# Kernel optimization log

Measured on AMD Instinct MI355X. Metric: run time of the kernel, lower is better.

The kernel has to match this reference:

```python
import jax, jax.numpy as jnp
import numpy as np

HIDDEN = 2048
NH = 32        # query heads
NKV = 4        # kv heads (GQA)
HD = 64        # head_dim
Q_SIZE = NH * HD      # 2048
KV_SIZE = NKV * HD    # 256
WINDOW = 1024         # sliding window size
THETA = 1000000.0
T = 2048              # tokens
SCALE = HD ** -0.5
NEG = -1e30


def setup_inputs() -> dict:
    key = jax.random.key(0)
    k1, k2, k3 = jax.random.split(key, 3)
    return {
        "positions": jnp.arange(T, dtype=jnp.int32),
        "hidden_states": jax.random.normal(k1, (T, HIDDEN), dtype=jnp.float32),
        "wqkv": jax.random.normal(k2, (HIDDEN, Q_SIZE + 2 * KV_SIZE), dtype=jnp.float32) * (HIDDEN ** -0.5),
        "wo": jax.random.normal(k3, (Q_SIZE, HIDDEN), dtype=jnp.float32) * (Q_SIZE ** -0.5),
    }


def _apply_rope(x, positions):
    # NeoX-style rotary embedding over full head_dim (rotate halves).
    half = HD // 2
    inv_freq = 1.0 / (THETA ** (jnp.arange(half, dtype=jnp.float32) / half))
    ang = positions.astype(jnp.float32)[:, None] * inv_freq[None, :]   # [T, half]
    cos = jnp.cos(ang)[:, None, :]   # [T, 1, half]
    sin = jnp.sin(ang)[:, None, :]
    x1, x2 = jnp.split(x, 2, axis=-1)
    return jnp.concatenate([x1 * cos - x2 * sin, x2 * cos + x1 * sin], axis=-1)


def reference(positions, hidden_states, wqkv, wo):
    # fused QKV projection
    qkv = hidden_states @ wqkv                          # [T, Q+2KV]
    q = qkv[:, :Q_SIZE].reshape(T, NH, HD)
    k = qkv[:, Q_SIZE:Q_SIZE + KV_SIZE].reshape(T, NKV, HD)
    v = qkv[:, Q_SIZE + KV_SIZE:].reshape(T, NKV, HD)
    # rotary embedding on q, k
    q = _apply_rope(q, positions)
    k = _apply_rope(k, positions)
    # GQA: repeat kv heads to match query heads
    group = NH // NKV
    kr = jnp.repeat(k, group, axis=1)                   # [T, NH, HD]
    vr = jnp.repeat(v, group, axis=1)
    scores = jnp.einsum('qhd,khd->hqk', q, kr) * SCALE  # [NH, T, T]
    # causal + sliding-window mask: attend to j in (i-WINDOW, i]
    i = jnp.arange(T)[:, None]
    j = jnp.arange(T)[None, :]
    mask = (j <= i) & (i - j < WINDOW)                  # [T, T]
    scores = jnp.where(mask[None, :, :], scores, NEG)
    probs = jax.nn.softmax(scores, axis=-1)
    attn = jnp.einsum('hqk,khd->qhd', probs, vr).reshape(T, Q_SIZE)
    return attn @ wo                                    # [T, HIDDEN]
```

## Files before the change

### kernel.cpp

```cpp
#include <hip/hip_runtime.h>
#include <hip/hip_bf16.h>

typedef float  f32x4  __attribute__((ext_vector_type(4)));
typedef __bf16 bf16x8 __attribute__((ext_vector_type(8)));
typedef __bf16 bf16x4 __attribute__((ext_vector_type(4)));
typedef __bf16 bf16x2 __attribute__((ext_vector_type(2)));

#define T_SEQ   2048
#define HIDDEN  2048
#define NH      32
#define NKV     4
#define HD      64
#define QSZ     2048
#define KVSZ    256
#define QKVN    2560
#define WINDOW  1024

#if __has_builtin(__builtin_amdgcn_exp2f)
#define EXPS(x) __builtin_amdgcn_exp2f(x)
#define QSCALE  0.1803368801111f
#else
#define EXPS(x) __expf(x)
#define QSCALE  0.125f
#endif

#define RAW_BARRIER()   asm volatile("s_barrier" ::: "memory")
#define WAITV(n)        asm volatile("s_waitcnt vmcnt(" #n ")" ::: "memory")

__device__ __forceinline__ void gll16(const __bf16* g, __bf16* l) {
    __builtin_amdgcn_global_load_lds(
        (const __attribute__((address_space(1))) void*)g,
        (__attribute__((address_space(3))) void*)l,
        16, 0, 0);
}

__global__ __launch_bounds__(256) void prep(const float4* __restrict__ hidden4,
                                            bf16x4* __restrict__ hidden_bf4,
                                            const float* __restrict__ wqkv,
                                            const float* __restrict__ wo,
                                            __bf16* __restrict__ wqkv_t,
                                            __bf16* __restrict__ wo_t,
                                            const int* __restrict__ pos,
                                            float2* __restrict__ ropetab) {
    __shared__ float tile[32][132];
    const int b = blockIdx.x;
    const int tid = threadIdx.x;

    if (b < 4096) {
        int id = b * 256 + tid;
        float4 v = hidden4[id];
        bf16x4 o;
        o[0] = (__bf16)v.x; o[1] = (__bf16)v.y; o[2] = (__bf16)v.z; o[3] = (__bf16)v.w;
        hidden_bf4[id] = o;
        return;
    }
    if (b < 4352) {
        int id = (b - 4096) * 256 + tid;
        int row = id >> 5, f = id & 31;
        float p = (float)pos[row];
        float ifr = exp2f((float)f * -0.62286151779138f);
        float sn, cs;
        sincosf(p * ifr, &sn, &cs);
        ropetab[id] = make_float2(cs, sn);
        return;
    }

    const float* in;
    __bf16* out;
    int Rin, Cin, bx, by;
    if (b < 5632) {
        int t = b - 4352;
        in = wqkv; out = wqkv_t; Rin = 2048; Cin = 2560;
        bx = t % 20; by = t / 20;
    } else {
        int t = b - 5632;
        in = wo; out = wo_t; Rin = 2048; Cin = 2048;
        bx = t % 16; by = t / 16;
    }
    const int ri = by * 32, ci = bx * 128;
    const int r0 = tid >> 5;
    const int c4 = tid & 31;
    #pragma unroll
    for (int i = 0; i < 4; i++) {
        float4 v = *reinterpret_cast<const float4*>(
            &in[(size_t)(ri + r0 + i * 8) * Cin + ci + c4 * 4]);
        *reinterpret_cast<float4*>(&tile[r0 + i * 8][c4 * 4]) = v;
    }
    __syncthreads();
    const int c  = tid >> 3;
    const int rb = tid & 7;
    #pragma unroll
    for (int j = 0; j < 4; j++) {
        int cc = c + j * 32;
        bf16x4 pk;
        #pragma unroll
        for (int i = 0; i < 4; i++) pk[i] = (__bf16)tile[rb * 4 + i][cc];
        *reinterpret_cast<bf16x4*>(&out[(size_t)(ci + cc) * Rin + ri + rb * 4]) = pk;
    }
}


#define GEMM_PROLOGUE_COMMON(Aptr, Btptr, Kdim)                                 \
    const int tid = threadIdx.x;                                                \
    const int wid = tid >> 6;                                                   \
    const int l   = tid & 63;                                                   \
    const int lg  = l >> 4;                                                     \
    const int ll  = l & 15;                                                     \
    const int swl = ll & 7;                                                     \
    const int wm  = wid >> 1, wn = wid & 1;                                     \
    const int gx   = gridDim.x;                                                 \
    const int flat = blockIdx.y * gx + blockIdx.x;                              \
    const int nwg  = gx * gridDim.y;                                            \
    const int swz  = (flat & 7) * (nwg >> 3) + (flat >> 3);                     \
    const int bm   = (swz / gx) * 64;                                           \
    const int bn   = (swz % gx) * 128;                                          \
    const __bf16* Ab = (Aptr) + (size_t)bm * (Kdim);                            \
    const __bf16* Bb = (Btptr) + (size_t)bn * (Kdim);                           \
    f32x4 acc[2][4];                                                            \
    _Pragma("unroll")                                                           \
    for (int i = 0; i < 2; i++)                                                 \
        _Pragma("unroll")                                                       \
        for (int j = 0; j < 4; j++)                                             \
            acc[i][j] = (f32x4){0.f, 0.f, 0.f, 0.f};                            \
    const int srow = tid >> 3;                                                  \
    const int sseg0 = tid & 7;

#define GEMM_STAGE(buf, k0, Kdim)                                               \
    {                                                                           \
        _Pragma("unroll")                                                       \
        for (int c = 0; c < 2; c++) {                                           \
            int row  = c * 32 + srow;                                           \
            int sseg = sseg0 ^ (row & 7);                                       \
            gll16(Ab + (size_t)row * (Kdim) + (k0) + sseg * 8,                  \
                  &Asm[buf][(c * 256 + tid) * 8]);                              \
        }                                                                       \
        _Pragma("unroll")                                                       \
        for (int c = 0; c < 4; c++) {                                           \
            int row  = c * 32 + srow;                                           \
            int sseg = sseg0 ^ (row & 7);                                       \
            gll16(Bb + (size_t)row * (Kdim) + (k0) + sseg * 8,                  \
                  &Bsm[buf][(c * 256 + tid) * 8]);                              \
        }                                                                       \
    }

#define GEMM_COMPUTE(bufidx)                                                    \
    _Pragma("unroll")                                                           \
    for (int ss = 0; ss < 2; ss++) {                                            \
        bf16x8 af[2], bfr[4];                                                   \
        _Pragma("unroll")                                                       \
        for (int mi = 0; mi < 2; mi++) {                                        \
            int r = wm * 32 + mi * 16 + ll;                                     \
            int u = (ss * 4 + lg) ^ swl;                                        \
            af[mi] = *reinterpret_cast<const bf16x8*>(&Asm[bufidx][r * 64 + u * 8]); \
        }                                                                       \
        _Pragma("unroll")                                                       \
        for (int ni = 0; ni < 4; ni++) {                                        \
            int r = wn * 64 + ni * 16 + ll;                                     \
            int u = (ss * 4 + lg) ^ swl;                                        \
            bfr[ni] = *reinterpret_cast<const bf16x8*>(&Bsm[bufidx][r * 64 + u * 8]); \
        }                                                                       \
        _Pragma("unroll")                                                       \
        for (int mi = 0; mi < 2; mi++)                                          \
            _Pragma("unroll")                                                   \
            for (int ni = 0; ni < 4; ni++)                                      \
                acc[mi][ni] = __builtin_amdgcn_mfma_f32_16x16x32_bf16(          \
                    af[mi], bfr[ni], acc[mi][ni], 0, 0, 0);                     \
    }

#define GEMM_KLOOP2(Kdim)                                                       \
    GEMM_STAGE(0, 0, Kdim)                                                      \
    int cur = 0;                                                                \
    for (int k0 = 0; k0 < (Kdim); k0 += 64) {                                   \
        RAW_BARRIER();                                                          \
        if (k0 + 64 < (Kdim)) {                                                 \
            GEMM_STAGE(cur ^ 1, k0 + 64, Kdim)                                  \
            WAITV(6);                                                           \
        } else {                                                                \
            WAITV(0);                                                           \
        }                                                                       \
        RAW_BARRIER();                                                          \
        __builtin_amdgcn_sched_barrier(0);                                      \
        GEMM_COMPUTE(cur)                                                       \
        cur ^= 1;                                                               \
    }

#define GEMM_KLOOP3(Kdim)                                                       \
    GEMM_STAGE(0, 0, Kdim)                                                      \
    GEMM_STAGE(1, 64, Kdim)                                                     \
    int cur = 0;                                                                \
    for (int k0 = 0; k0 < (Kdim); k0 += 64) {                                   \
        if (k0 + 64 < (Kdim)) { WAITV(6); } else { WAITV(0); }                  \
        RAW_BARRIER();                                                          \
        __builtin_amdgcn_sched_barrier(0);                                      \
        if (k0 + 128 < (Kdim)) {                                                \
            int nb = cur + 2; if (nb >= 3) nb -= 3;                             \
            GEMM_STAGE(nb, k0 + 128, Kdim)                                      \
        }                                                                       \
        GEMM_COMPUTE(cur)                                                       \
        cur = (cur == 2) ? 0 : cur + 1;                                         \
    }

__global__ __launch_bounds__(256) void gemm_out(const __bf16* __restrict__ A,
                                                const __bf16* __restrict__ Bt,
                                                float* __restrict__ Cout,
                                                int M, int N, int K) {
    __shared__ __align__(16) __bf16 Asm[3][64 * 64];
    __shared__ __align__(16) __bf16 Bsm[3][128 * 64];
    GEMM_PROLOGUE_COMMON(A, Bt, K)
    GEMM_KLOOP3(K)
    #pragma unroll
    for (int mi = 0; mi < 2; mi++)
        #pragma unroll
        for (int ni = 0; ni < 4; ni++)
            #pragma unroll
            for (int r = 0; r < 4; r++) {
                int row = bm + wm*32 + mi*16 + lg*4 + r;
                int col = bn + wn*64 + ni*16 + ll;
                Cout[(size_t)row * N + col] = acc[mi][ni][r];
            }
}

__global__ __launch_bounds__(256) void gemm_qkv(const __bf16* __restrict__ A,
                                                const __bf16* __restrict__ Bt,
                                                const float2* __restrict__ ropetab,
                                                __bf16* __restrict__ q,
                                                __bf16* __restrict__ k,
                                                __bf16* __restrict__ vT) {
    __shared__ __align__(16) __bf16 Asm[2][64 * 64];
    __shared__ __align__(16) __bf16 Bsm[2][128 * 64];
    GEMM_PROLOGUE_COMMON(A, Bt, HIDDEN)
    GEMM_KLOOP2(HIDDEN)

    if (bn < QSZ + KVSZ) {
        const bool isq = (bn < QSZ);
        #pragma unroll
        for (int mi = 0; mi < 2; mi++) {
            #pragma unroll
            for (int r = 0; r < 4; r++) {
                int row = bm + wm*32 + mi*16 + lg*4 + r;
                const float2* tb = &ropetab[row * 32 + ll];
                #pragma unroll
                for (int ni = 0; ni < 2; ni++) {
                    float2 cssn = tb[ni * 16];
                    float x1 = acc[mi][ni][r], x2 = acc[mi][ni + 2][r];
                    float o1 = x1 * cssn.x - x2 * cssn.y;
                    float o2 = x2 * cssn.x + x1 * cssn.y;
                    int col = bn + wn*64 + ni*16 + ll;
                    if (isq) {
                        q[(size_t)row * QSZ + col]      = (__bf16)(o1 * QSCALE);
                        q[(size_t)row * QSZ + col + 32] = (__bf16)(o2 * QSCALE);
                    } else {
                        k[(size_t)row * KVSZ + (col - QSZ)]      = (__bf16)o1;
                        k[(size_t)row * KVSZ + (col - QSZ) + 32] = (__bf16)o2;
                    }
                }
            }
        }
    } else {
        #pragma unroll
        for (int mi = 0; mi < 2; mi++) {
            int row0 = bm + wm*32 + mi*16 + lg*4;
            #pragma unroll
            for (int ni = 0; ni < 4; ni++) {
                int d = bn + wn*64 + ni*16 + ll - (QSZ + KVSZ);
                bf16x4 pk;
                #pragma unroll
                for (int r = 0; r < 4; r++) pk[r] = (__bf16)acc[mi][ni][r];
                *reinterpret_cast<bf16x4*>(&vT[(size_t)d * T_SEQ + row0]) = pk;
            }
        }
    }
}

__global__ __launch_bounds__(512) void attn_kernel(const __bf16* __restrict__ qg,
                                                   const __bf16* __restrict__ kgl,
                                                   const __bf16* __restrict__ vTg,
                                                   __bf16* __restrict__ og) {
    const int qb  = blockIdx.x;
    const int hp  = blockIdx.y;
    const int kvh = hp >> 2;
    const int tid = threadIdx.x;
    const int wid = tid >> 6;
    const int h   = hp * 2 + (wid >> 2);
    const int l   = tid & 63;
    const int lg  = l >> 4;
    const int ll  = l & 15;
    const int i0  = qb * 64;
    const int qw  = i0 + (wid & 3) * 16;
    const int qi  = qw + ll;

    __shared__ __align__(16) __bf16 Ksm[3][64 * 64];
    __shared__ __align__(16) __bf16 VTs[3][64 * 64];

    bf16x8 qf[2];
    {
        const __bf16* qp = qg + (size_t)(qw + ll) * QSZ + h * 64 + lg * 8;
        qf[0] = *reinterpret_cast<const bf16x8*>(qp);
        qf[1] = *reinterpret_cast<const bf16x8*>(qp + 32);
    }

    f32x4 o[4];
    #pragma unroll
    for (int dn = 0; dn < 4; dn++) o[dn] = (f32x4){0.f, 0.f, 0.f, 0.f};
    float l_run = 0.f;

    int jlo = i0 - (WINDOW - 1); if (jlo < 0) jlo = 0;
    int t0v = jlo & ~63;
    int tend = i0 + 64;

    const int srow = tid >> 3;
    const int sg   = (tid & 7) ^ (srow & 7);
    const int krow = (srow & 35) | ((srow & 8) << 1) | ((srow & 4) << 1) | ((srow & 16) >> 2);
    const __bf16* kp = kgl + (size_t)krow * KVSZ + kvh * 64 + sg * 8;
    const __bf16* vp = vTg + (size_t)(kvh * 64 + srow) * T_SEQ + sg * 8;

#define ASTAGE(buf, t)                                      \
    {                                                       \
        gll16(kp + (size_t)(t) * KVSZ, &Ksm[buf][tid * 8]); \
        gll16(vp + (t),                &VTs[buf][tid * 8]); \
    }

    ASTAGE(0, t0v);
    if (t0v + 64 < tend) ASTAGE(1, t0v + 64);

    const int swl = ll & 7;
    const int u0 = (lg ^ swl) * 8;
    const int u1 = ((4 + lg) ^ swl) * 8;

    int cur = 0;
    for (int t = t0v; t < tend; t += 64) {
        if (t + 64 < tend) { WAITV(2); } else { WAITV(0); }
        RAW_BARRIER();
        __builtin_amdgcn_sched_barrier(0);
        if (t + 128 < tend) {
            int nb = cur + 2; if (nb >= 3) nb -= 3;
            ASTAGE(nb, t + 128);
        }

        bool active = (t <= qw + 15) && (t + 63 >= qw - (WINDOW - 1));
        if (active) {
            f32x4 sT[4];
            __builtin_amdgcn_s_setprio(1);
            #pragma unroll
            for (int kt = 0; kt < 4; kt++) {
                sT[kt] = (f32x4){0.f, 0.f, 0.f, 0.f};
                bf16x8 kf0 = *reinterpret_cast<const bf16x8*>(&Ksm[cur][kt*1024 + ll*64 + u0]);
                sT[kt] = __builtin_amdgcn_mfma_f32_16x16x32_bf16(kf0, qf[0], sT[kt], 0, 0, 0);
                bf16x8 kf1 = *reinterpret_cast<const bf16x8*>(&Ksm[cur][kt*1024 + ll*64 + u1]);
                sT[kt] = __builtin_amdgcn_mfma_f32_16x16x32_bf16(kf1, qf[1], sT[kt], 0, 0, 0);
            }
            __builtin_amdgcn_s_setprio(0);

            bool full = (t + 63 <= qw) && (t >= qw + 15 - (WINDOW - 1));
            float ts = 0.f;
            if (full) {
                #pragma unroll
                for (int kt = 0; kt < 4; kt++) {
                    #pragma unroll
                    for (int r = 0; r < 4; r++) {
                        float p = EXPS(sT[kt][r]);
                        sT[kt][r] = p;
                        ts += p;
                    }
                }
            } else {
                #pragma unroll
                for (int kt = 0; kt < 4; kt++) {
                    int jb = t + ((kt & 2) << 4) + ((kt & 1) << 2) + (lg << 3);
                    #pragma unroll
                    for (int r = 0; r < 4; r++) {
                        int j = jb + r;
                        bool ok = (j <= qi) && (qi - j < WINDOW);
                        float p = ok ? EXPS(sT[kt][r]) : 0.f;
                        sT[kt][r] = p;
                        ts += p;
                    }
                }
            }
            ts += __shfl_xor(ts, 16);
            ts += __shfl_xor(ts, 32);
            l_run += ts;

            __builtin_amdgcn_s_setprio(1);
            #pragma unroll
            for (int kt2 = 0; kt2 < 2; kt2++) {
                bf16x8 pa;
                #pragma unroll
                for (int r = 0; r < 4; r++) {
                    pa[r]     = (__bf16)sT[kt2*2][r];
                    pa[r + 4] = (__bf16)sT[kt2*2 + 1][r];
                }
                int uv = kt2 ? u1 : u0;
                #pragma unroll
                for (int dn = 0; dn < 4; dn++) {
                    bf16x8 vf = *reinterpret_cast<const bf16x8*>(&VTs[cur][dn*1024 + ll*64 + uv]);
                    o[dn] = __builtin_amdgcn_mfma_f32_16x16x32_bf16(pa, vf, o[dn], 0, 0, 0);
                }
            }
            __builtin_amdgcn_s_setprio(0);
        }
        cur = (cur == 2) ? 0 : cur + 1;
    }
#undef ASTAGE

    float linv = 1.0f / l_run;
    float i0v = __shfl(linv, lg*4 + 0);
    float i1v = __shfl(linv, lg*4 + 1);
    float i2v = __shfl(linv, lg*4 + 2);
    float i3v = __shfl(linv, lg*4 + 3);
    #pragma unroll
    for (int dn = 0; dn < 4; dn++) {
        og[(size_t)(qw + lg*4 + 0) * QSZ + h*64 + dn*16 + ll] = (__bf16)(o[dn][0] * i0v);
        og[(size_t)(qw + lg*4 + 1) * QSZ + h*64 + dn*16 + ll] = (__bf16)(o[dn][1] * i1v);
        og[(size_t)(qw + lg*4 + 2) * QSZ + h*64 + dn*16 + ll] = (__bf16)(o[dn][2] * i2v);
        og[(size_t)(qw + lg*4 + 3) * QSZ + h*64 + dn*16 + ll] = (__bf16)(o[dn][3] * i3v);
    }
}

extern "C" void kernel_launch(void* const* d_in, const int* in_sizes, int n_in,
                              void* d_out, int out_size, void* d_ws, size_t ws_size,
                              hipStream_t stream) {
    const int*   positions = (const int*)d_in[0];
    const float* hidden    = (const float*)d_in[1];
    const float* wqkv      = (const float*)d_in[2];
    const float* wo        = (const float*)d_in[3];
    float* out = (float*)d_out;

    char* ws = (char*)d_ws;
    __bf16* hidden_bf = (__bf16*)(ws);
    __bf16* wqkv_t    = (__bf16*)(ws + 8388608);
    __bf16* wo_t      = (__bf16*)(ws + 18874368);
    __bf16* q_bf      = (__bf16*)(ws + 37748736);
    __bf16* k_bf      = (__bf16*)(ws + 46137344);
    __bf16* vT_bf     = (__bf16*)(ws + 47185920);
    __bf16* attn_bf   = (__bf16*)(ws + 48234496);
    float2* ropetab   = (float2*)(ws + 56623104);

    prep<<<dim3(6656), dim3(256), 0, stream>>>(
        (const float4*)hidden, (bf16x4*)hidden_bf, wqkv, wo,
        wqkv_t, wo_t, positions, ropetab);

    gemm_qkv<<<dim3(QKVN / 128, T_SEQ / 64), dim3(256), 0, stream>>>(
        hidden_bf, wqkv_t, ropetab, q_bf, k_bf, vT_bf);

    attn_kernel<<<dim3(T_SEQ / 64, 16), dim3(512), 0, stream>>>(
        q_bf, k_bf, vT_bf, attn_bf);

    gemm_out<<<dim3(HIDDEN / 128, T_SEQ / 64), dim3(256), 0, stream>>>(
        attn_bf, wo_t, out, T_SEQ, HIDDEN, QSZ);
}
```

Measured before the change: 106.1 us.

## Move wo transpose-convert into attention launch as extra blocks

The wo fp32-to-bf16 transpose leaves the prep kernel and runs as 1024 extra blocks appended to the attention grid. The attention kernel now uses one flat grid and a shared memory buffer that both roles carve up. The aim is to overlap the bandwidth-bound weight conversion with compute-bound attention and shorten the prep launch. The risk is that the extra blocks compete for CUs with attention blocks and change the tail behaviour.

```diff
diff --git a/kernel.cpp b/kernel.cpp
--- a/kernel.cpp
+++ b/kernel.cpp
@@ -37,9 +37,7 @@
 __global__ __launch_bounds__(256) void prep(const float4* __restrict__ hidden4,
                                             bf16x4* __restrict__ hidden_bf4,
                                             const float* __restrict__ wqkv,
-                                            const float* __restrict__ wo,
                                             __bf16* __restrict__ wqkv_t,
-                                            __bf16* __restrict__ wo_t,
                                             const int* __restrict__ pos,
                                             float2* __restrict__ ropetab) {
     __shared__ float tile[32][132];
@@ -65,25 +63,15 @@
         return;
     }
 
-    const float* in;
-    __bf16* out;
-    int Rin, Cin, bx, by;
-    if (b < 5632) {
-        int t = b - 4352;
-        in = wqkv; out = wqkv_t; Rin = 2048; Cin = 2560;
-        bx = t % 20; by = t / 20;
-    } else {
-        int t = b - 5632;
-        in = wo; out = wo_t; Rin = 2048; Cin = 2048;
-        bx = t % 16; by = t / 16;
-    }
+    int t = b - 4352;
+    const int bx = t % 20, by = t / 20;
     const int ri = by * 32, ci = bx * 128;
     const int r0 = tid >> 5;
     const int c4 = tid & 31;
     #pragma unroll
     for (int i = 0; i < 4; i++) {
         float4 v = *reinterpret_cast<const float4*>(
-            &in[(size_t)(ri + r0 + i * 8) * Cin + ci + c4 * 4]);
+            &wqkv[(size_t)(ri + r0 + i * 8) * QKVN + ci + c4 * 4]);
         *reinterpret_cast<float4*>(&tile[r0 + i * 8][c4 * 4]) = v;
     }
     __syncthreads();
@@ -95,7 +83,7 @@
         bf16x4 pk;
         #pragma unroll
         for (int i = 0; i < 4; i++) pk[i] = (__bf16)tile[rb * 4 + i][cc];
-        *reinterpret_cast<bf16x4*>(&out[(size_t)(ci + cc) * Rin + ri + rb * 4]) = pk;
+        *reinterpret_cast<bf16x4*>(&wqkv_t[(size_t)(ci + cc) * HIDDEN + ri + rb * 4]) = pk;
     }
 }
 
@@ -272,14 +260,52 @@
     }
 }
 
-__global__ __launch_bounds__(512) void attn_kernel(const __bf16* __restrict__ qg,
-                                                   const __bf16* __restrict__ kgl,
-                                                   const __bf16* __restrict__ vTg,
-                                                   __bf16* __restrict__ og) {
-    const int qb  = blockIdx.x;
-    const int hp  = blockIdx.y;
+__global__ __launch_bounds__(512) void attn_fused(const __bf16* __restrict__ qg,
+                                                  const __bf16* __restrict__ kgl,
+                                                  const __bf16* __restrict__ vTg,
+                                                  __bf16* __restrict__ og,
+                                                  const float* __restrict__ wo,
+                                                  __bf16* __restrict__ wo_t) {
+    __shared__ __align__(16) char smem[49152];
+    const int b   = blockIdx.x;
+    const int tid = threadIdx.x;
+
+    if (b >= 512) {
+        float (*tile)[132] = (float(*)[132])smem;
+        int t = b - 512;
+        const int bx = t & 15, by = t >> 4;
+        const int ri = by * 32, ci = bx * 128;
+        const int r0 = tid >> 4;
+        const int c8 = tid & 15;
+        #pragma unroll
+        for (int j = 0; j < 2; j++) {
+            int col = c8 * 8 + j * 4;
+            float4 v = *reinterpret_cast<const float4*>(
+                &wo[(size_t)(ri + r0) * HIDDEN + ci + col]);
+            *reinterpret_cast<float4*>(&tile[r0][col]) = v;
+        }
+        __syncthreads();
+        #pragma unroll
+        for (int j = 0; j < 2; j++) {
+            int u  = tid + j * 512;
+            int cc = u >> 3;
+            int rb = u & 7;
+            bf16x4 pk;
+            #pragma unroll
+            for (int i = 0; i < 4; i++) pk[i] = (__bf16)tile[rb * 4 + i][cc];
+            *reinterpret_cast<bf16x4*>(&wo_t[(size_t)(ci + cc) * HIDDEN + ri + rb * 4]) = pk;
+        }
+        return;
+    }
+
+    __bf16* Ksm = (__bf16*)smem;
+    __bf16* VTs = (__bf16*)(smem + 24576);
+#define KSM(buf) (Ksm + (buf) * 4096)
+#define VSM(buf) (VTs + (buf) * 4096)
+
+    const int qb  = b & 31;
+    const int hp  = b >> 5;
     const int kvh = hp >> 2;
-    const int tid = threadIdx.x;
     const int wid = tid >> 6;
     const int h   = hp * 2 + (wid >> 2);
     const int l   = tid & 63;
@@ -289,9 +315,6 @@
     const int qw  = i0 + (wid & 3) * 16;
     const int qi  = qw + ll;
 
-    __shared__ __align__(16) __bf16 Ksm[3][64 * 64];
-    __shared__ __align__(16) __bf16 VTs[3][64 * 64];
-
     bf16x8 qf[2];
     {
         const __bf16* qp = qg + (size_t)(qw + ll) * QSZ + h * 64 + lg * 8;
@@ -314,10 +337,10 @@
     const __bf16* kp = kgl + (size_t)krow * KVSZ + kvh * 64 + sg * 8;
     const __bf16* vp = vTg + (size_t)(kvh * 64 + srow) * T_SEQ + sg * 8;
 
-#define ASTAGE(buf, t)                                      \
-    {                                                       \
-        gll16(kp + (size_t)(t) * KVSZ, &Ksm[buf][tid * 8]); \
-        gll16(vp + (t),                &VTs[buf][tid * 8]); \
+#define ASTAGE(buf, t)                                   \
+    {                                                    \
+        gll16(kp + (size_t)(t) * KVSZ, KSM(buf) + tid * 8); \
+        gll16(vp + (t),                VSM(buf) + tid * 8); \
     }
 
     ASTAGE(0, t0v);
@@ -344,9 +367,9 @@
             #pragma unroll
             for (int kt = 0; kt < 4; kt++) {
                 sT[kt] = (f32x4){0.f, 0.f, 0.f, 0.f};
-                bf16x8 kf0 = *reinterpret_cast<const bf16x8*>(&Ksm[cur][kt*1024 + ll*64 + u0]);
+                bf16x8 kf0 = *reinterpret_cast<const bf16x8*>(KSM(cur) + kt*1024 + ll*64 + u0);
                 sT[kt] = __builtin_amdgcn_mfma_f32_16x16x32_bf16(kf0, qf[0], sT[kt], 0, 0, 0);
-                bf16x8 kf1 = *reinterpret_cast<const bf16x8*>(&Ksm[cur][kt*1024 + ll*64 + u1]);
+                bf16x8 kf1 = *reinterpret_cast<const bf16x8*>(KSM(cur) + kt*1024 + ll*64 + u1);
                 sT[kt] = __builtin_amdgcn_mfma_f32_16x16x32_bf16(kf1, qf[1], sT[kt], 0, 0, 0);
             }
             __builtin_amdgcn_s_setprio(0);
@@ -393,7 +416,7 @@
                 int uv = kt2 ? u1 : u0;
                 #pragma unroll
                 for (int dn = 0; dn < 4; dn++) {
-                    bf16x8 vf = *reinterpret_cast<const bf16x8*>(&VTs[cur][dn*1024 + ll*64 + uv]);
+                    bf16x8 vf = *reinterpret_cast<const bf16x8*>(VSM(cur) + dn*1024 + ll*64 + uv);
                     o[dn] = __builtin_amdgcn_mfma_f32_16x16x32_bf16(pa, vf, o[dn], 0, 0, 0);
                 }
             }
@@ -402,6 +425,8 @@
         cur = (cur == 2) ? 0 : cur + 1;
     }
 #undef ASTAGE
+#undef KSM
+#undef VSM
 
     float linv = 1.0f / l_run;
     float i0v = __shfl(linv, lg*4 + 0);
@@ -436,15 +461,14 @@
     __bf16* attn_bf   = (__bf16*)(ws + 48234496);
     float2* ropetab   = (float2*)(ws + 56623104);
 
-    prep<<<dim3(6656), dim3(256), 0, stream>>>(
-        (const float4*)hidden, (bf16x4*)hidden_bf, wqkv, wo,
-        wqkv_t, wo_t, positions, ropetab);
+    prep<<<dim3(5632), dim3(256), 0, stream>>>(
+        (const float4*)hidden, (bf16x4*)hidden_bf, wqkv, wqkv_t, positions, ropetab);
 
     gemm_qkv<<<dim3(QKVN / 128, T_SEQ / 64), dim3(256), 0, stream>>>(
         hidden_bf, wqkv_t, ropetab, q_bf, k_bf, vT_bf);
 
-    attn_kernel<<<dim3(T_SEQ / 64, 16), dim3(512), 0, stream>>>(
-        q_bf, k_bf, vT_bf, attn_bf);
+    attn_fused<<<dim3(1536), dim3(512), 0, stream>>>(
+        q_bf, k_bf, vT_bf, attn_bf, wo, wo_t);
 
     gemm_out<<<dim3(HIDDEN / 128, T_SEQ / 64), dim3(256), 0, stream>>>(
         attn_bf, wo_t, out, T_SEQ, HIDDEN, QSZ);
```

New measurement: 102.0 us (median of 3 runs). 3.9% less time.
